# Performance work log

Hardware: AMD Instinct MI355X
Metric: run time of the kernel (lower is better)

The kernel has to match this reference:

```python
import jax, jax.numpy as jnp
import numpy as np

N = 4096        # n_locations
D_MODEL = 512
H, D_K, D_V = 4, 128, 256


def setup_inputs() -> dict:
    key = jax.random.key(0)
    ks = jax.random.split(key, 7)
    s = 0.02
    return {
        "Q": jax.random.normal(ks[0], (N, D_MODEL), dtype=jnp.float32),
        "K": jax.random.normal(ks[1], (N, D_MODEL), dtype=jnp.float32),
        "V": jax.random.normal(ks[2], (N, D_MODEL), dtype=jnp.float32),
        "Wq": jax.random.normal(ks[3], (H, D_MODEL, D_K), dtype=jnp.float32) * s,
        "Wk": jax.random.normal(ks[4], (H, D_MODEL, D_K), dtype=jnp.float32) * s,
        "Wv": jax.random.normal(ks[5], (H, D_MODEL, D_V), dtype=jnp.float32) * s,
        "Wo": jax.random.normal(ks[6], (D_MODEL, H * D_V), dtype=jnp.float32) * s,
    }


def reference(Q, K, V, Wq, Wk, Wv, Wo):
    n = K.shape[0]
    # Batched per-head projections: [h, n, d_k] / [h, n, d_v]
    q = jnp.einsum('nd,hdk->hnk', Q, Wq)
    k = jnp.einsum('nd,hdk->hnk', K, Wk)
    v = jnp.einsum('nd,hdv->hnv', V, Wv)
    # NOTE: original scales by sqrt(n_locations) (K.size(0)), not sqrt(d_k)
    scores = jnp.einsum('hqk,hnk->hqn', q, k) / jnp.sqrt(jnp.asarray(n, q.dtype))
    weights = jax.nn.softmax(scores, axis=-1)          # [h, n, n]
    heads = jnp.einsum('hqn,hnv->hqv', weights, v)      # [h, n, d_v]
    # concat heads along feature dim: [n, h*d_v]
    x = jnp.transpose(heads, (1, 0, 2)).reshape(heads.shape[1], -1)
    return x @ Wo.T                                     # [n, d_model]
```

## Files before the change

kernel.cpp:

```cpp
#include <hip/hip_runtime.h>
#include <hip/hip_bf16.h>
#include <type_traits>

typedef __hip_bfloat16 bf16;
typedef __attribute__((ext_vector_type(8))) short bf16x8;
typedef __attribute__((ext_vector_type(4))) float f32x4;

#define N_LOC 4096

__device__ __forceinline__ bf16 to_bf16(float f) { return __float2bfloat16(f); }

__device__ __forceinline__ void dma16(const bf16* g, bf16* l) {
  __builtin_amdgcn_global_load_lds((const __attribute__((address_space(1))) unsigned int*)g,
                                   (__attribute__((address_space(3))) unsigned int*)l, 16, 0, 0);
}

__global__ __launch_bounds__(256) void prep(const float* __restrict__ Q, const float* __restrict__ K,
                                            const float* __restrict__ V, const float* __restrict__ Wo,
                                            bf16* __restrict__ Qb, bf16* __restrict__ Kb,
                                            bf16* __restrict__ Vb, bf16* __restrict__ Wob,
                                            const float* __restrict__ Wq, const float* __restrict__ Wk,
                                            const float* __restrict__ Wv,
                                            bf16* __restrict__ oq, bf16* __restrict__ ok,
                                            bf16* __restrict__ ov) {
  __shared__ float tile[64][65];
  if (blockIdx.x < 3328) {
    long i = ((long)blockIdx.x * 256 + threadIdx.x) * 8;
    const float* src;
    bf16* dst;
    long off;
    if (i < 2097152)      { src = Q;  dst = Qb;  off = i; }
    else if (i < 4194304) { src = K;  dst = Kb;  off = i - 2097152; }
    else if (i < 6291456) { src = V;  dst = Vb;  off = i - 4194304; }
    else                  { src = Wo; dst = Wob; off = i - 6291456; }
    float4 a = *(const float4*)&src[off];
    float4 b = *(const float4*)&src[off + 4];
    union { bf16 h[8]; bf16x8 v; } u;
    u.h[0] = to_bf16(a.x); u.h[1] = to_bf16(a.y); u.h[2] = to_bf16(a.z); u.h[3] = to_bf16(a.w);
    u.h[4] = to_bf16(b.x); u.h[5] = to_bf16(b.y); u.h[6] = to_bf16(b.z); u.h[7] = to_bf16(b.w);
    *(bf16x8*)&dst[off] = u.v;
  } else {
    int pid = blockIdx.x - 3328;
    int z = pid >> 7;
    int rem = pid & 127;
    int xx = rem & 7, y = rem >> 3;
    const float* W = (z == 0) ? Wq : (z == 1) ? Wk : Wv;
    bf16* out = (z == 0) ? oq : (z == 1) ? ok : ov;
    int DH = (z == 2) ? 256 : 128;
    int nt = DH >> 6;
    if (y >= 4 * nt) return;
    int h = y / nt, tt = y - h * nt;
    int d0 = xx * 64, t0 = tt * 64;
    for (int i = threadIdx.x; i < 4096; i += 256) {
      int r = i >> 6, c = i & 63;
      tile[r][c] = W[((size_t)h * 512 + d0 + r) * DH + t0 + c];
    }
    __syncthreads();
    for (int i = threadIdx.x; i < 4096; i += 256) {
      int t = i >> 6, d = i & 63;
      out[((size_t)(h * DH + t0 + t)) * 512 + d0 + d] = to_bf16(tile[d][t]);
    }
  }
}

template <int BN, int MODE, typename OutT>
__device__ __forceinline__ void gemm_body(const bf16* __restrict__ A, const bf16* __restrict__ Bt,
                                          OutT* __restrict__ C, int N, int K, int m0, int n0,
                                          bf16* sm) {
  constexpr int WN = BN / 2, JN = WN / 16, NB = BN / 32;
  int tid = threadIdx.x, lane = tid & 63, w = tid >> 6;
  int quad = lane >> 4, l16 = lane & 15;
  int wm = (w >> 1) * 64, wn = (w & 1) * WN;
  int srow = lane >> 3;
  int sG = (lane & 7) ^ srow;

  bf16* Asb[2] = { sm, sm + 8192 };
  bf16* Bsb[2] = { sm + 16384, sm + 16384 + BN * 64 };

  const bf16* ga[4];
  const bf16* gb[NB];
#pragma unroll
  for (int j = 0; j < 4; j++) ga[j] = A + (long)(m0 + (4 * j + w) * 8 + srow) * K + sG * 8;
#pragma unroll
  for (int j = 0; j < NB; j++) gb[j] = Bt + (long)(n0 + (4 * j + w) * 8 + srow) * K + sG * 8;

  auto stage = [&](int b) {
#pragma unroll
    for (int j = 0; j < 4; j++) { dma16(ga[j], &Asb[b][(4 * j + w) * 512]); ga[j] += 64; }
#pragma unroll
    for (int j = 0; j < NB; j++) { dma16(gb[j], &Bsb[b][(4 * j + w) * 512]); gb[j] += 64; }
  };

  f32x4 acc[4][JN] = {};
  stage(0);
  asm volatile("" ::: "memory");
  int cur = 0;
  const int NK = K >> 6;
  for (int s = 0; s < NK; ++s) {
    if (s + 1 < NK) {
      stage(cur ^ 1);
      if constexpr (NB == 4)      asm volatile("s_waitcnt vmcnt(8)" ::: "memory");
      else if constexpr (NB == 2) asm volatile("s_waitcnt vmcnt(6)" ::: "memory");
      else                        asm volatile("s_waitcnt vmcnt(5)" ::: "memory");
    } else {
      asm volatile("s_waitcnt vmcnt(0)" ::: "memory");
    }
    __builtin_amdgcn_s_barrier();
    asm volatile("" ::: "memory");
    const bf16* Ac = Asb[cur];
    const bf16* Bc = Bsb[cur];
#pragma unroll
    for (int kk = 0; kk < 2; kk++) {
      bf16x8 af[4], bfr[JN];
#pragma unroll
      for (int i = 0; i < 4; i++) {
        int r = wm + i * 16 + l16;
        af[i] = *(const bf16x8*)&Ac[r * 64 + (((kk * 4 + quad) ^ r) & 7) * 8];
      }
#pragma unroll
      for (int j = 0; j < JN; j++) {
        int r = wn + j * 16 + l16;
        bfr[j] = *(const bf16x8*)&Bc[r * 64 + (((kk * 4 + quad) ^ r) & 7) * 8];
      }
#pragma unroll
      for (int i = 0; i < 4; i++)
#pragma unroll
        for (int j = 0; j < JN; j++)
          acc[i][j] = __builtin_amdgcn_mfma_f32_16x16x32_bf16(af[i], bfr[j], acc[i][j], 0, 0, 0);
    }
    asm volatile("" ::: "memory");
    __builtin_amdgcn_s_barrier();
    asm volatile("" ::: "memory");
    cur ^= 1;
  }

  if constexpr (MODE == 2) {
    bf16* tp = sm;
#pragma unroll
    for (int i = 0; i < 4; i++)
#pragma unroll
      for (int j = 0; j < JN; j++)
#pragma unroll
        for (int r = 0; r < 4; r++)
          tp[(wn + j * 16 + l16) * 136 + wm + i * 16 + quad * 4 + r] = to_bf16(acc[i][j][r]);
    __syncthreads();
#pragma unroll
    for (int it = 0; it < 8; ++it) {
      int idx = it * 256 + tid;
      int rown = idx >> 4, c8 = (idx & 15) * 8;
      *(bf16x8*)&C[(size_t)(n0 + rown) * 4096 + m0 + c8] = *(const bf16x8*)&tp[rown * 136 + c8];
    }
  } else {
#pragma unroll
    for (int i = 0; i < 4; i++)
#pragma unroll
      for (int j = 0; j < JN; j++)
#pragma unroll
        for (int r = 0; r < 4; r++) {
          long row = m0 + wm + i * 16 + quad * 4 + r;
          long col = n0 + wn + j * 16 + l16;
          if constexpr (MODE == 0)
            C[row * N + col] = to_bf16(acc[i][j][r]);
          else
            C[row * N + col] = acc[i][j][r];
        }
  }
}

__global__ __launch_bounds__(256) void proj_gemm(const bf16* __restrict__ QKVb,
                                                 const bf16* __restrict__ Wt,
                                                 bf16* __restrict__ qkout,
                                                 bf16* __restrict__ vTout) {
  __shared__ __align__(16) bf16 sm[4 * 128 * 64];
  int bid = blockIdx.x;
  if (bid < 256) {
    int z = bid >> 7;
    int t = bid & 127;
    int g = t & 7, r = t >> 3;
    int m0 = (g * 4 + (r & 3)) * 128;
    int n0 = (r >> 2) * 128;
    gemm_body<128, 0, bf16>(QKVb + (size_t)z * 2097152, Wt + (size_t)z * 262144,
                            qkout + (size_t)z * 2097152, 512, 512, m0, n0, sm);
  } else {
    int t = bid - 256;
    int g = t & 7, r = t >> 3;
    int m0 = (g * 4 + (r & 3)) * 128;
    int n0 = (r >> 2) * 128;
    gemm_body<128, 2, bf16>(QKVb + (size_t)2 * 2097152, Wt + (size_t)2 * 262144,
                            vTout, 1024, 512, m0, n0, sm);
  }
}

__global__ __launch_bounds__(256) void out_gemm(const bf16* __restrict__ xin,
                                                const bf16* __restrict__ Wob,
                                                float* __restrict__ outp) {
  __shared__ __align__(16) bf16 sm[2 * 128 * 64 + 2 * 32 * 64];
  int bid = blockIdx.x;
  int g = bid & 7, r = bid >> 3;
  int m0 = (g * 4 + (r & 3)) * 128;
  int n0 = (r >> 2) * 32;
  gemm_body<32, 1, float>(xin, Wob, outp, 512, 1024, m0, n0, sm);
}

__global__ __launch_bounds__(512, 4) void attn(const bf16* __restrict__ qb,
                                               const bf16* __restrict__ kb,
                                               const bf16* __restrict__ vT,
                                               bf16* __restrict__ x) {
  __shared__ __align__(16) bf16 kt[2][64 * 128];
  __shared__ __align__(16) bf16 vt[2][128 * 64];
  __shared__ __align__(16) bf16 pt[64 * 72];
  __shared__ float Lrow[64];

  const int bid = blockIdx.x;
  const int xcd = bid & 7;
  const int head = xcd & 3;
  const int dvh = xcd >> 2;
  const int q0 = (bid >> 3) * 64;
  const int tid = threadIdx.x;
  const int lane = tid & 63, w = tid >> 6;
  const int quad = lane >> 4, l16 = lane & 15;
  const int cd = w & 3;
  const int g = w >> 2;

  bf16x8 onesf;
  {
    union { bf16 h[8]; bf16x8 v; } u;
    bf16 one = to_bf16(1.0f), zero = to_bf16(0.0f);
#pragma unroll
    for (int j = 0; j < 8; j++) u.h[j] = (l16 == 0) ? one : zero;
    onesf = u.v;
  }

  bf16x8 qf[2][4];
#pragma unroll
  for (int i = 0; i < 2; i++) {
    const bf16* qrow = &qb[(size_t)(q0 + g * 32 + i * 16 + l16) * 512 + head * 128];
#pragma unroll
    for (int kk = 0; kk < 4; kk++) qf[i][kk] = *(const bf16x8*)&qrow[kk * 32 + quad * 8];
  }

  f32x4 oacc[2][2] = {};
  f32x4 oL[2] = {};
  const float scale = 1.0f / 64.0f;

  const int j0 = 2 * w, j1 = 2 * w + 1;
  const bf16 *kp0, *kp1, *vp0, *vp1;
  {
    int r0 = 4 * j0 + (lane >> 4), r1 = 4 * j1 + (lane >> 4);
    int p = lane & 15;
    int G0 = (p & 8) | ((p ^ r0) & 7), G1 = (p & 8) | ((p ^ r1) & 7);
    kp0 = kb + (size_t)r0 * 512 + head * 128 + G0 * 8;
    kp1 = kb + (size_t)r1 * 512 + head * 128 + G1 * 8;
  }
  {
    int r0 = 8 * j0 + (lane >> 3), r1 = 8 * j1 + (lane >> 3);
    int p = lane & 7;
    int G0 = (p ^ r0) & 7, G1 = (p ^ r1) & 7;
    vp0 = vT + (size_t)(head * 256 + dvh * 128 + r0) * 4096 + G0 * 8;
    vp1 = vT + (size_t)(head * 256 + dvh * 128 + r1) * 4096 + G1 * 8;
  }

#define STAGE_K(b)                                      \
  do {                                                  \
    dma16(kp0, &kt[b][j0 * 512]);                       \
    dma16(kp1, &kt[b][j1 * 512]);                       \
    kp0 += 64 * 512; kp1 += 64 * 512;                   \
  } while (0)
#define STAGE_V(b)                                      \
  do {                                                  \
    dma16(vp0, &vt[b][j0 * 512]);                       \
    dma16(vp1, &vt[b][j1 * 512]);                       \
    vp0 += 64; vp1 += 64;                               \
  } while (0)

  STAGE_K(0);
  STAGE_V(0);
  STAGE_K(1);
  asm volatile("s_waitcnt vmcnt(2)" ::: "memory");
  __builtin_amdgcn_s_barrier();
  asm volatile("" ::: "memory");
  {
    const bf16* ktc = kt[0];
    f32x4 sacc[2] = {};
#pragma unroll
    for (int kk = 0; kk < 4; kk++) {
      int R = cd * 16 + l16;
      int G = kk * 4 + quad;
      bf16x8 kf = *(const bf16x8*)&ktc[R * 128 + (((G ^ R) & 7) | (G & 8)) * 8];
      sacc[0] = __builtin_amdgcn_mfma_f32_16x16x32_bf16(qf[0][kk], kf, sacc[0], 0, 0, 0);
      sacc[1] = __builtin_amdgcn_mfma_f32_16x16x32_bf16(qf[1][kk], kf, sacc[1], 0, 0, 0);
    }
#pragma unroll
    for (int i = 0; i < 2; i++)
#pragma unroll
      for (int r = 0; r < 4; r++)
        pt[(g * 32 + i * 16 + quad * 4 + r) * 72 + cd * 16 + l16] =
            to_bf16(__expf(sacc[i][r] * scale));
  }
  asm volatile("s_waitcnt lgkmcnt(0)" ::: "memory");
  __builtin_amdgcn_s_barrier();
  asm volatile("" ::: "memory");

  for (int t = 0; t < 64; ++t) {
    bf16x8 pf[2][2];
#pragma unroll
    for (int kk = 0; kk < 2; kk++)
#pragma unroll
      for (int i = 0; i < 2; i++)
        pf[kk][i] = *(const bf16x8*)&pt[(g * 32 + i * 16 + l16) * 72 + kk * 32 + quad * 8];
    asm volatile("s_waitcnt lgkmcnt(0)" ::: "memory");
    __builtin_amdgcn_s_barrier();
    asm volatile("" ::: "memory");

    if (t < 62) STAGE_K(t & 1);
    if (t < 63) STAGE_V((t + 1) & 1);
    if (t < 62)      asm volatile("s_waitcnt vmcnt(4)" ::: "memory");
    else if (t == 62) asm volatile("s_waitcnt vmcnt(2)" ::: "memory");
    else              asm volatile("s_waitcnt vmcnt(0)" ::: "memory");

    if (t < 63) {
      const bf16* ktc = kt[(t + 1) & 1];
      const bf16* vtc = vt[t & 1];
      f32x4 sacc[2] = {};
#pragma unroll
      for (int kk = 0; kk < 4; kk++) {
        int R = cd * 16 + l16;
        int G = kk * 4 + quad;
        bf16x8 kf = *(const bf16x8*)&ktc[R * 128 + (((G ^ R) & 7) | (G & 8)) * 8];
        sacc[0] = __builtin_amdgcn_mfma_f32_16x16x32_bf16(qf[0][kk], kf, sacc[0], 0, 0, 0);
        sacc[1] = __builtin_amdgcn_mfma_f32_16x16x32_bf16(qf[1][kk], kf, sacc[1], 0, 0, 0);
      }
#pragma unroll
      for (int kk = 0; kk < 2; kk++) {
#pragma unroll
        for (int c = 0; c < 2; c++) {
          int R = cd * 32 + c * 16 + l16;
          int G = kk * 4 + quad;
          bf16x8 vf = *(const bf16x8*)&vtc[R * 64 + ((G ^ R) & 7) * 8];
#pragma unroll
          for (int i = 0; i < 2; i++)
            oacc[i][c] = __builtin_amdgcn_mfma_f32_16x16x32_bf16(pf[kk][i], vf, oacc[i][c], 0, 0, 0);
        }
        if (cd == 3) {
#pragma unroll
          for (int i = 0; i < 2; i++)
            oL[i] = __builtin_amdgcn_mfma_f32_16x16x32_bf16(pf[kk][i], onesf, oL[i], 0, 0, 0);
        }
      }
#pragma unroll
      for (int i = 0; i < 2; i++)
#pragma unroll
        for (int r = 0; r < 4; r++)
          pt[(g * 32 + i * 16 + quad * 4 + r) * 72 + cd * 16 + l16] =
              to_bf16(__expf(sacc[i][r] * scale));
    } else {
      const bf16* vtc = vt[t & 1];
#pragma unroll
      for (int kk = 0; kk < 2; kk++) {
#pragma unroll
        for (int c = 0; c < 2; c++) {
          int R = cd * 32 + c * 16 + l16;
          int G = kk * 4 + quad;
          bf16x8 vf = *(const bf16x8*)&vtc[R * 64 + ((G ^ R) & 7) * 8];
#pragma unroll
          for (int i = 0; i < 2; i++)
            oacc[i][c] = __builtin_amdgcn_mfma_f32_16x16x32_bf16(pf[kk][i], vf, oacc[i][c], 0, 0, 0);
        }
        if (cd == 3) {
#pragma unroll
          for (int i = 0; i < 2; i++)
            oL[i] = __builtin_amdgcn_mfma_f32_16x16x32_bf16(pf[kk][i], onesf, oL[i], 0, 0, 0);
        }
      }
    }
    asm volatile("s_waitcnt lgkmcnt(0)" ::: "memory");
    __builtin_amdgcn_s_barrier();
    asm volatile("" ::: "memory");
  }
#undef STAGE_K
#undef STAGE_V

  if (cd == 3 && l16 == 0) {
#pragma unroll
    for (int i = 0; i < 2; i++)
#pragma unroll
      for (int r = 0; r < 4; r++) Lrow[g * 32 + i * 16 + quad * 4 + r] = oL[i][r];
  }
  __syncthreads();

#pragma unroll
  for (int i = 0; i < 2; i++)
#pragma unroll
    for (int c = 0; c < 2; c++)
#pragma unroll
      for (int r = 0; r < 4; r++) {
        int row = g * 32 + i * 16 + quad * 4 + r;
        float v = oacc[i][c][r] / Lrow[row];
        x[(size_t)(q0 + row) * 1024 + head * 256 + dvh * 128 + cd * 32 + c * 16 + l16] =
            to_bf16(v);
      }
}

extern "C" void kernel_launch(void* const* d_in, const int* in_sizes, int n_in,
                              void* d_out, int out_size, void* d_ws, size_t ws_size,
                              hipStream_t stream) {
  const float* Q  = (const float*)d_in[0];
  const float* Km = (const float*)d_in[1];
  const float* V  = (const float*)d_in[2];
  const float* Wq = (const float*)d_in[3];
  const float* Wk = (const float*)d_in[4];
  const float* Wv = (const float*)d_in[5];
  const float* Wo = (const float*)d_in[6];
  float* out = (float*)d_out;

  bf16* ws  = (bf16*)d_ws;
  bf16* Qb  = ws;
  bf16* Kb  = Qb + 2097152;
  bf16* Vb  = Kb + 2097152;
  bf16* Wqt = Vb + 2097152;
  bf16* Wkt = Wqt + 262144;
  bf16* Wvt = Wkt + 262144;
  bf16* Wob = Wvt + 524288;
  bf16* qb  = Wob + 524288;
  bf16* kb  = qb + 2097152;
  bf16* vT  = kb + 2097152;
  bf16* x   = vT + 4194304;

  prep<<<3712, 256, 0, stream>>>(Q, Km, V, Wo, Qb, Kb, Vb, Wob, Wq, Wk, Wv, Wqt, Wkt, Wvt);

  proj_gemm<<<512, 256, 0, stream>>>(Qb, Wqt, qb, vT);

  attn<<<512, 512, 0, stream>>>(qb, kb, vT, x);

  out_gemm<<<512, 256, 0, stream>>>(x, Wob, out);
}
```

Measured before the change: 217.2 us.

## Fuse fp32-to-bf16 input conversion into GEMM tile loads, drop separate cast pass

The prep kernel no longer casts Q, K, V and Wo to bf16. The projection and output GEMMs now read the fp32 operands directly, convert them in registers and store them to LDS instead of using the global-to-LDS DMA path. This removes a full read and write pass over about 26 MB of activations. In exchange, the A or B loads become synchronous register loads, and an extra lgkmcnt wait is added before each barrier. The out_gemm tile also changes from BN=32 to BN=64 on a 2D grid with 256 blocks, and the XCD-aware block swizzle is removed.

Result: no change. 216.1 us (-0.5%).

```diff
diff --git a/kernel.cpp b/kernel.cpp
--- a/kernel.cpp
+++ b/kernel.cpp
@@ -15,59 +15,39 @@
                                    (__attribute__((address_space(3))) unsigned int*)l, 16, 0, 0);
 }
 
-__global__ __launch_bounds__(256) void prep(const float* __restrict__ Q, const float* __restrict__ K,
-                                            const float* __restrict__ V, const float* __restrict__ Wo,
-                                            bf16* __restrict__ Qb, bf16* __restrict__ Kb,
-                                            bf16* __restrict__ Vb, bf16* __restrict__ Wob,
-                                            const float* __restrict__ Wq, const float* __restrict__ Wk,
+__global__ __launch_bounds__(256) void prep(const float* __restrict__ Wq, const float* __restrict__ Wk,
                                             const float* __restrict__ Wv,
                                             bf16* __restrict__ oq, bf16* __restrict__ ok,
                                             bf16* __restrict__ ov) {
   __shared__ float tile[64][65];
-  if (blockIdx.x < 3328) {
-    long i = ((long)blockIdx.x * 256 + threadIdx.x) * 8;
-    const float* src;
-    bf16* dst;
-    long off;
-    if (i < 2097152)      { src = Q;  dst = Qb;  off = i; }
-    else if (i < 4194304) { src = K;  dst = Kb;  off = i - 2097152; }
-    else if (i < 6291456) { src = V;  dst = Vb;  off = i - 4194304; }
-    else                  { src = Wo; dst = Wob; off = i - 6291456; }
-    float4 a = *(const float4*)&src[off];
-    float4 b = *(const float4*)&src[off + 4];
-    union { bf16 h[8]; bf16x8 v; } u;
-    u.h[0] = to_bf16(a.x); u.h[1] = to_bf16(a.y); u.h[2] = to_bf16(a.z); u.h[3] = to_bf16(a.w);
-    u.h[4] = to_bf16(b.x); u.h[5] = to_bf16(b.y); u.h[6] = to_bf16(b.z); u.h[7] = to_bf16(b.w);
-    *(bf16x8*)&dst[off] = u.v;
-  } else {
-    int pid = blockIdx.x - 3328;
-    int z = pid >> 7;
-    int rem = pid & 127;
-    int xx = rem & 7, y = rem >> 3;
-    const float* W = (z == 0) ? Wq : (z == 1) ? Wk : Wv;
-    bf16* out = (z == 0) ? oq : (z == 1) ? ok : ov;
-    int DH = (z == 2) ? 256 : 128;
-    int nt = DH >> 6;
-    if (y >= 4 * nt) return;
-    int h = y / nt, tt = y - h * nt;
-    int d0 = xx * 64, t0 = tt * 64;
-    for (int i = threadIdx.x; i < 4096; i += 256) {
-      int r = i >> 6, c = i & 63;
-      tile[r][c] = W[((size_t)h * 512 + d0 + r) * DH + t0 + c];
-    }
-    __syncthreads();
-    for (int i = threadIdx.x; i < 4096; i += 256) {
-      int t = i >> 6, d = i & 63;
-      out[((size_t)(h * DH + t0 + t)) * 512 + d0 + d] = to_bf16(tile[d][t]);
-    }
-  }
-}
-
-template <int BN, int MODE, typename OutT>
-__device__ __forceinline__ void gemm_body(const bf16* __restrict__ A, const bf16* __restrict__ Bt,
+  int pid = blockIdx.x;
+  int z = pid >> 7;
+  int rem = pid & 127;
+  int xx = rem & 7, y = rem >> 3;
+  const float* W = (z == 0) ? Wq : (z == 1) ? Wk : Wv;
+  bf16* out = (z == 0) ? oq : (z == 1) ? ok : ov;
+  int DH = (z == 2) ? 256 : 128;
+  int nt = DH >> 6;
+  if (y >= 4 * nt) return;
+  int h = y / nt, tt = y - h * nt;
+  int d0 = xx * 64, t0 = tt * 64;
+  for (int i = threadIdx.x; i < 4096; i += 256) {
+    int r = i >> 6, c = i & 63;
+    tile[r][c] = W[((size_t)h * 512 + d0 + r) * DH + t0 + c];
+  }
+  __syncthreads();
+  for (int i = threadIdx.x; i < 4096; i += 256) {
+    int t = i >> 6, d = i & 63;
+    out[((size_t)(h * DH + t0 + t)) * 512 + d0 + d] = to_bf16(tile[d][t]);
+  }
+}
+
+template <int BN, int MODE, bool F32A, bool F32B, typename OutT>
+__device__ __forceinline__ void gemm_body(const void* __restrict__ Av, const void* __restrict__ Btv,
                                           OutT* __restrict__ C, int N, int K, int m0, int n0,
                                           bf16* sm) {
   constexpr int WN = BN / 2, JN = WN / 16, NB = BN / 32;
+  constexpr int NDMA = (F32A ? 0 : 4) + (F32B ? 0 : NB);
   int tid = threadIdx.x, lane = tid & 63, w = tid >> 6;
   int quad = lane >> 4, l16 = lane & 15;
   int wm = (w >> 1) * 64, wn = (w & 1) * WN;
@@ -77,18 +57,47 @@
   bf16* Asb[2] = { sm, sm + 8192 };
   bf16* Bsb[2] = { sm + 16384, sm + 16384 + BN * 64 };
 
-  const bf16* ga[4];
-  const bf16* gb[NB];
-#pragma unroll
-  for (int j = 0; j < 4; j++) ga[j] = A + (long)(m0 + (4 * j + w) * 8 + srow) * K + sG * 8;
-#pragma unroll
-  for (int j = 0; j < NB; j++) gb[j] = Bt + (long)(n0 + (4 * j + w) * 8 + srow) * K + sG * 8;
+  const bf16* Ab = (const bf16*)Av;
+  const float* Af = (const float*)Av;
+  const bf16* Bb = (const bf16*)Btv;
+  const float* Bf = (const float*)Btv;
+
+  long aoff[4];
+  long boff[NB];
+#pragma unroll
+  for (int j = 0; j < 4; j++) aoff[j] = (long)(m0 + (4 * j + w) * 8 + srow) * K + sG * 8;
+#pragma unroll
+  for (int j = 0; j < NB; j++) boff[j] = (long)(n0 + (4 * j + w) * 8 + srow) * K + sG * 8;
 
   auto stage = [&](int b) {
 #pragma unroll
-    for (int j = 0; j < 4; j++) { dma16(ga[j], &Asb[b][(4 * j + w) * 512]); ga[j] += 64; }
-#pragma unroll
-    for (int j = 0; j < NB; j++) { dma16(gb[j], &Bsb[b][(4 * j + w) * 512]); gb[j] += 64; }
+    for (int j = 0; j < 4; j++) {
+      if constexpr (F32A) {
+        float4 xa = *(const float4*)&Af[aoff[j]];
+        float4 xb = *(const float4*)&Af[aoff[j] + 4];
+        union { bf16 h[8]; bf16x8 v; } u;
+        u.h[0] = to_bf16(xa.x); u.h[1] = to_bf16(xa.y); u.h[2] = to_bf16(xa.z); u.h[3] = to_bf16(xa.w);
+        u.h[4] = to_bf16(xb.x); u.h[5] = to_bf16(xb.y); u.h[6] = to_bf16(xb.z); u.h[7] = to_bf16(xb.w);
+        *(bf16x8*)&Asb[b][(4 * j + w) * 512 + lane * 8] = u.v;
+      } else {
+        dma16(&Ab[aoff[j]], &Asb[b][(4 * j + w) * 512]);
+      }
+      aoff[j] += 64;
+    }
+#pragma unroll
+    for (int j = 0; j < NB; j++) {
+      if constexpr (F32B) {
+        float4 xa = *(const float4*)&Bf[boff[j]];
+        float4 xb = *(const float4*)&Bf[boff[j] + 4];
+        union { bf16 h[8]; bf16x8 v; } u;
+        u.h[0] = to_bf16(xa.x); u.h[1] = to_bf16(xa.y); u.h[2] = to_bf16(xa.z); u.h[3] = to_bf16(xa.w);
+        u.h[4] = to_bf16(xb.x); u.h[5] = to_bf16(xb.y); u.h[6] = to_bf16(xb.z); u.h[7] = to_bf16(xb.w);
+        *(bf16x8*)&Bsb[b][(4 * j + w) * 512 + lane * 8] = u.v;
+      } else {
+        dma16(&Bb[boff[j]], &Bsb[b][(4 * j + w) * 512]);
+      }
+      boff[j] += 64;
+    }
   };
 
   f32x4 acc[4][JN] = {};
@@ -99,12 +108,16 @@
   for (int s = 0; s < NK; ++s) {
     if (s + 1 < NK) {
       stage(cur ^ 1);
-      if constexpr (NB == 4)      asm volatile("s_waitcnt vmcnt(8)" ::: "memory");
-      else if constexpr (NB == 2) asm volatile("s_waitcnt vmcnt(6)" ::: "memory");
-      else                        asm volatile("s_waitcnt vmcnt(5)" ::: "memory");
+      if constexpr (NDMA == 8)      asm volatile("s_waitcnt vmcnt(8)" ::: "memory");
+      else if constexpr (NDMA == 6) asm volatile("s_waitcnt vmcnt(6)" ::: "memory");
+      else if constexpr (NDMA == 5) asm volatile("s_waitcnt vmcnt(5)" ::: "memory");
+      else if constexpr (NDMA == 4) asm volatile("s_waitcnt vmcnt(4)" ::: "memory");
+      else if constexpr (NDMA == 2) asm volatile("s_waitcnt vmcnt(2)" ::: "memory");
+      else                          asm volatile("s_waitcnt vmcnt(0)" ::: "memory");
     } else {
       asm volatile("s_waitcnt vmcnt(0)" ::: "memory");
     }
+    asm volatile("s_waitcnt lgkmcnt(0)" ::: "memory");
     __builtin_amdgcn_s_barrier();
     asm volatile("" ::: "memory");
     const bf16* Ac = Asb[cur];
@@ -167,7 +180,9 @@
   }
 }
 
-__global__ __launch_bounds__(256) void proj_gemm(const bf16* __restrict__ QKVb,
+__global__ __launch_bounds__(256) void proj_gemm(const float* __restrict__ Q,
+                                                 const float* __restrict__ Kin,
+                                                 const float* __restrict__ V,
                                                  const bf16* __restrict__ Wt,
                                                  bf16* __restrict__ qkout,
                                                  bf16* __restrict__ vTout) {
@@ -176,30 +191,24 @@
   if (bid < 256) {
     int z = bid >> 7;
     int t = bid & 127;
-    int g = t & 7, r = t >> 3;
-    int m0 = (g * 4 + (r & 3)) * 128;
-    int n0 = (r >> 2) * 128;
-    gemm_body<128, 0, bf16>(QKVb + (size_t)z * 2097152, Wt + (size_t)z * 262144,
-                            qkout + (size_t)z * 2097152, 512, 512, m0, n0, sm);
+    int m0 = (t & 31) * 128, n0 = (t >> 5) * 128;
+    const float* A = (z == 0) ? Q : Kin;
+    gemm_body<128, 0, true, false, bf16>(A, Wt + (size_t)z * 262144,
+                                         qkout + (size_t)z * 2097152, 512, 512, m0, n0, sm);
   } else {
     int t = bid - 256;
-    int g = t & 7, r = t >> 3;
-    int m0 = (g * 4 + (r & 3)) * 128;
-    int n0 = (r >> 2) * 128;
-    gemm_body<128, 2, bf16>(QKVb + (size_t)2 * 2097152, Wt + (size_t)2 * 262144,
-                            vTout, 1024, 512, m0, n0, sm);
+    int m0 = (t & 31) * 128, n0 = (t >> 5) * 128;
+    gemm_body<128, 2, true, false, bf16>(V, Wt + (size_t)2 * 262144,
+                                         vTout, 1024, 512, m0, n0, sm);
   }
 }
 
 __global__ __launch_bounds__(256) void out_gemm(const bf16* __restrict__ xin,
-                                                const bf16* __restrict__ Wob,
+                                                const float* __restrict__ Wo,
                                                 float* __restrict__ outp) {
-  __shared__ __align__(16) bf16 sm[2 * 128 * 64 + 2 * 32 * 64];
-  int bid = blockIdx.x;
-  int g = bid & 7, r = bid >> 3;
-  int m0 = (g * 4 + (r & 3)) * 128;
-  int n0 = (r >> 2) * 32;
-  gemm_body<32, 1, float>(xin, Wob, outp, 512, 1024, m0, n0, sm);
+  __shared__ __align__(16) bf16 sm[2 * 128 * 64 + 2 * 64 * 64];
+  gemm_body<64, 1, false, true, float>(xin, Wo, outp, 512, 1024,
+                                       blockIdx.x * 128, blockIdx.y * 64, sm);
 }
 
 __global__ __launch_bounds__(512, 4) void attn(const bf16* __restrict__ qb,
@@ -414,23 +423,19 @@
   float* out = (float*)d_out;
 
   bf16* ws  = (bf16*)d_ws;
-  bf16* Qb  = ws;
-  bf16* Kb  = Qb + 2097152;
-  bf16* Vb  = Kb + 2097152;
-  bf16* Wqt = Vb + 2097152;
+  bf16* Wqt = ws;
   bf16* Wkt = Wqt + 262144;
   bf16* Wvt = Wkt + 262144;
-  bf16* Wob = Wvt + 524288;
-  bf16* qb  = Wob + 524288;
+  bf16* qb  = Wvt + 524288;
   bf16* kb  = qb + 2097152;
   bf16* vT  = kb + 2097152;
   bf16* x   = vT + 4194304;
 
-  prep<<<3712, 256, 0, stream>>>(Q, Km, V, Wo, Qb, Kb, Vb, Wob, Wq, Wk, Wv, Wqt, Wkt, Wvt);
-
-  proj_gemm<<<512, 256, 0, stream>>>(Qb, Wqt, qb, vT);
+  prep<<<384, 256, 0, stream>>>(Wq, Wk, Wv, Wqt, Wkt, Wvt);
+
+  proj_gemm<<<512, 256, 0, stream>>>(Q, Km, V, Wqt, qb, vT);
 
   attn<<<512, 512, 0, stream>>>(qb, kb, vT, x);
 
-  out_gemm<<<512, 256, 0, stream>>>(x, Wob, out);
-}
+  out_gemm<<<dim3(32, 8), 256, 0, stream>>>(x, Wo, out);
+}
```
